# Optimization experiments

Measured on AMD Instinct MI355X. Metric: run time of the kernel, lower is better.

Reference implementation:

```python
import jax, jax.numpy as jnp
import numpy as np

D_MODEL = 1024
D_STATE = 16
D_CONV = 4
EXPAND = 2
D_INNER = EXPAND * D_MODEL          # 2048
DT_RANK = (D_MODEL + 15) // 16      # 64 = ceil(d_model/16)
B, L = 1, 2048


def setup_inputs() -> dict:
    key = jax.random.key(0)
    ks = jax.random.split(key, 8)
    s = lambda fan_in: 1.0 / np.sqrt(fan_in)
    x = jax.random.normal(ks[0], (B, L, D_MODEL), dtype=jnp.float32)
    in_proj_w = jax.random.normal(ks[1], (2 * D_INNER, D_MODEL), dtype=jnp.float32) * s(D_MODEL)
    conv_w = jax.random.normal(ks[2], (D_INNER, 1, D_CONV), dtype=jnp.float32) * s(D_CONV)
    conv_b = jax.random.normal(ks[3], (D_INNER,), dtype=jnp.float32) * s(D_CONV)
    x_proj_w = jax.random.normal(ks[4], (DT_RANK + 2 * D_STATE, D_INNER), dtype=jnp.float32) * s(D_INNER)
    dt_proj_w = jax.random.normal(ks[5], (D_INNER, DT_RANK), dtype=jnp.float32) * s(DT_RANK)
    dt_proj_b = jax.random.normal(ks[6], (D_INNER,), dtype=jnp.float32) * s(DT_RANK)
    A_log = jnp.log(jnp.arange(1, D_STATE + 1, dtype=jnp.float32))[None, :] * jnp.ones((D_INNER, 1), jnp.float32)
    D_param = jnp.ones((D_INNER,), dtype=jnp.float32)
    out_proj_w = jax.random.normal(ks[7], (D_MODEL, D_INNER), dtype=jnp.float32) * s(D_INNER)
    return {"x": x, "in_proj_w": in_proj_w, "conv_w": conv_w, "conv_b": conv_b,
            "x_proj_w": x_proj_w, "dt_proj_w": dt_proj_w, "dt_proj_b": dt_proj_b,
            "A_log": A_log, "D_param": D_param, "out_proj_w": out_proj_w}


def _silu(v):
    return v * jax.nn.sigmoid(v)


def _mamba_fwd(x, in_proj_w, conv_w, conv_b, x_proj_w, dt_proj_w, dt_proj_b, A_log, D_param, out_proj_w):
    b, l, _ = x.shape
    d_state = A_log.shape[1]
    dt_rank = dt_proj_w.shape[1]
    # input projection and gate split
    xz = x @ in_proj_w.T                         # [B, L, 2*d_inner]
    x_inner, z = jnp.split(xz, 2, axis=-1)
    # causal depthwise conv (torch pads both sides then slices [:L] -> left pad only)
    x_c = jax.lax.conv_general_dilated(
        x_inner.transpose(0, 2, 1), conv_w,
        window_strides=(1,), padding=[(conv_w.shape[-1] - 1, 0)],
        feature_group_count=x_inner.shape[-1],
        dimension_numbers=('NCH', 'OIH', 'NCH'))
    x_conv = _silu((x_c + conv_b[None, :, None]).transpose(0, 2, 1))   # [B, L, d_inner]
    # SSM parameterization
    x_dbl = x_conv @ x_proj_w.T                  # [B, L, dt_rank + 2*d_state]
    dt_lr = x_dbl[..., :dt_rank]
    B_ssm = x_dbl[..., dt_rank:dt_rank + d_state]            # [B, L, n]
    C_ssm = x_dbl[..., dt_rank + d_state:]                   # [B, L, n]
    dt = jax.nn.softplus(dt_lr @ dt_proj_w.T + dt_proj_b)    # [B, L, d_inner]
    A = -jnp.exp(A_log)                                      # [d_inner, n]
    dA = jnp.exp(jnp.einsum('bld,dn->bldn', dt, A))          # [B, L, d_inner, n]
    dBx = jnp.einsum('bld,bln->bldn', dt * x_conv, B_ssm)    # dB * x_conv
    # selective scan over time
    def step(h, inp):
        a_t, bx_t, c_t = inp                                 # [B,d,n], [B,d,n], [B,n]
        h = a_t * h + bx_t
        y_t = jnp.einsum('bdn,bn->bd', h, c_t)
        return h, y_t
    h0 = jnp.zeros((b, x_conv.shape[-1], d_state), dtype=x.dtype)
    _, ys = jax.lax.scan(step, h0,
                         (dA.transpose(1, 0, 2, 3), dBx.transpose(1, 0, 2, 3),
                          C_ssm.transpose(1, 0, 2)))
    y = ys.transpose(1, 0, 2) + x_conv * D_param             # [B, L, d_inner]
    return (y * _silu(z)) @ out_proj_w.T                     # [B, L, d_model]


def reference(x, in_proj_w, conv_w, conv_b, x_proj_w, dt_proj_w, dt_proj_b, A_log, D_param, out_proj_w):
    return _mamba_fwd(x, in_proj_w, conv_w, conv_b, x_proj_w, dt_proj_w, dt_proj_b, A_log, D_param, out_proj_w)
```

## Files before the change

### kernel.cpp

```cpp
#include <hip/hip_runtime.h>

#define L_SEQ   2048
#define DMODEL  1024
#define DINNER  2048
#define DSTATE  16
#define RANK    64
#define NPROJ   96
#define NPAD    128
#define XZDIM   4096
#define CHUNK   32
#define NCHUNK  64
#define SPLITK  8

typedef __bf16 bf16x8 __attribute__((ext_vector_type(8)));
typedef float  f32x4  __attribute__((ext_vector_type(4)));

__device__ __forceinline__ unsigned short f2bf(float f) {
  unsigned int x = __float_as_uint(f);
  x += 0x7FFF + ((x >> 16) & 1);
  return (unsigned short)(x >> 16);
}

#define GLD16(g, l)                                                            \
  __builtin_amdgcn_global_load_lds(                                            \
      (const __attribute__((address_space(1))) void*)(g),                      \
      (__attribute__((address_space(3))) void*)(l), 16, 0, 0)

__global__ __launch_bounds__(256) void f32_to_bf16_kernel(
    const float* __restrict__ src, unsigned short* __restrict__ dst) {
  size_t i = ((size_t)blockIdx.x * 256 + threadIdx.x) * 8;
  float4 v0 = *(const float4*)(src + i);
  float4 v1 = *(const float4*)(src + i + 4);
  unsigned short o[8];
  o[0] = f2bf(v0.x); o[1] = f2bf(v0.y); o[2] = f2bf(v0.z); o[3] = f2bf(v0.w);
  o[4] = f2bf(v1.x); o[5] = f2bf(v1.y); o[6] = f2bf(v1.z); o[7] = f2bf(v1.w);
  *(ushort4*)(dst + i)     = make_ushort4(o[0], o[1], o[2], o[3]);
  *(ushort4*)(dst + i + 4) = make_ushort4(o[4], o[5], o[6], o[7]);
}

__global__ __launch_bounds__(256) void pad_convert_xw_kernel(
    const float* __restrict__ src, unsigned short* __restrict__ dst) {
  size_t i = ((size_t)blockIdx.x * 256 + threadIdx.x) * 8;
  int row = (int)(i >> 11);
  unsigned short o[8];
  if (row < NPROJ) {
    float4 v0 = *(const float4*)(src + i);
    float4 v1 = *(const float4*)(src + i + 4);
    o[0] = f2bf(v0.x); o[1] = f2bf(v0.y); o[2] = f2bf(v0.z); o[3] = f2bf(v0.w);
    o[4] = f2bf(v1.x); o[5] = f2bf(v1.y); o[6] = f2bf(v1.z); o[7] = f2bf(v1.w);
  } else {
    for (int t = 0; t < 8; t++) o[t] = 0;
  }
  *(ushort4*)(dst + i)     = make_ushort4(o[0], o[1], o[2], o[3]);
  *(ushort4*)(dst + i + 4) = make_ushort4(o[4], o[5], o[6], o[7]);
}

template <int BM, int BN, int WM, int WN>
__global__ __launch_bounds__(256) void gemm_tile(
    const unsigned short* __restrict__ A, const unsigned short* __restrict__ B,
    float* __restrict__ C, int M, int N, int K) {
  constexpr int WGN = BN / WN;
  constexpr int FM = WM / 16, FN = WN / 16;
  constexpr int CA = BM * 4 / 256;
  constexpr int CB = BN * 4 / 256;
  __shared__ unsigned short As[BM * 32];
  __shared__ unsigned short Bs[BN * 32];
  const int tid  = threadIdx.x;
  const int lane = tid & 63;
  const int wave = tid >> 6;
  const int wr = wave / WGN, wc = wave % WGN;
  const int fr = lane & 15;
  const int kq = (lane >> 4) * 8;
  const size_t bm = blockIdx.y, bn = blockIdx.x;

  f32x4 acc[FM][FN] = {};

  const unsigned short* aptr[CA];
  const unsigned short* bptr[CB];
#pragma unroll
  for (int i = 0; i < CA; i++) {
    int q = tid + i * 256;
    aptr[i] = A + (bm * BM + (q >> 2)) * (size_t)K + (q & 3) * 8;
  }
#pragma unroll
  for (int i = 0; i < CB; i++) {
    int q = tid + i * 256;
    bptr[i] = B + (bn * BN + (q >> 2)) * (size_t)K + (q & 3) * 8;
  }

  for (int k0 = 0; k0 < K; k0 += 32) {
#pragma unroll
    for (int i = 0; i < CA; i++) GLD16(aptr[i] + k0, &As[(tid + i * 256) * 8]);
#pragma unroll
    for (int i = 0; i < CB; i++) GLD16(bptr[i] + k0, &Bs[(tid + i * 256) * 8]);
    __syncthreads();
    bf16x8 af[FM], bg[FN];
#pragma unroll
    for (int m = 0; m < FM; m++)
      af[m] = *(const bf16x8*)&As[(wr * WM + m * 16 + fr) * 32 + kq];
#pragma unroll
    for (int n = 0; n < FN; n++)
      bg[n] = *(const bf16x8*)&Bs[(wc * WN + n * 16 + fr) * 32 + kq];
#pragma unroll
    for (int m = 0; m < FM; m++)
#pragma unroll
      for (int n = 0; n < FN; n++)
        acc[m][n] = __builtin_amdgcn_mfma_f32_16x16x32_bf16(af[m], bg[n],
                                                            acc[m][n], 0, 0, 0);
    __syncthreads();
  }
  const int cr = (lane >> 4) * 4;
#pragma unroll
  for (int m = 0; m < FM; m++)
#pragma unroll
    for (int n = 0; n < FN; n++) {
      float* cp = C + (bm * BM + wr * WM + m * 16 + cr) * (size_t)N +
                  bn * BN + wc * WN + n * 16 + fr;
#pragma unroll
      for (int r = 0; r < 4; r++) cp[(size_t)r * N] = acc[m][n][r];
    }
}

__global__ __launch_bounds__(256) void gemm_dt64_bf16(
    const unsigned short* __restrict__ A,
    const unsigned short* __restrict__ B,
    const float* __restrict__ bias,
    float* __restrict__ dt) {
  __shared__ unsigned short As[64 * 32];
  __shared__ unsigned short Bs[64 * 32];
  const int K = RANK;
  const int tid  = threadIdx.x;
  const int lane = tid & 63;
  const int wave = tid >> 6;
  const int wr = wave >> 1, wc = wave & 1;
  const int fr = lane & 15;
  const int kq = (lane >> 4) * 8;
  const size_t bm = blockIdx.y, bn = blockIdx.x;

  f32x4 acc[2][2] = {};

  const unsigned short* a0 = A + (bm * 64 + (tid >> 2)) * (size_t)K + (tid & 3) * 8;
  const unsigned short* b0 = B + (bn * 64 + (tid >> 2)) * (size_t)K + (tid & 3) * 8;

  for (int k0 = 0; k0 < K; k0 += 32) {
    GLD16(a0 + k0, &As[tid * 8]);
    GLD16(b0 + k0, &Bs[tid * 8]);
    __syncthreads();
    bf16x8 af[2], bg[2];
#pragma unroll
    for (int m = 0; m < 2; m++)
      af[m] = *(const bf16x8*)&As[(wr * 32 + m * 16 + fr) * 32 + kq];
#pragma unroll
    for (int n = 0; n < 2; n++)
      bg[n] = *(const bf16x8*)&Bs[(wc * 32 + n * 16 + fr) * 32 + kq];
#pragma unroll
    for (int m = 0; m < 2; m++)
#pragma unroll
      for (int n = 0; n < 2; n++)
        acc[m][n] = __builtin_amdgcn_mfma_f32_16x16x32_bf16(af[m], bg[n],
                                                            acc[m][n], 0, 0, 0);
    __syncthreads();
  }
  const int cr = (lane >> 4) * 4;
#pragma unroll
  for (int n = 0; n < 2; n++) {
    int col = (int)bn * 64 + wc * 32 + n * 16 + fr;
    float bv = bias[col];
#pragma unroll
    for (int m = 0; m < 2; m++) {
      float* cp = dt + ((size_t)bm * 64 + wr * 32 + m * 16 + cr) * DINNER + col;
#pragma unroll
      for (int r = 0; r < 4; r++) {
        float a = acc[m][n][r] + bv;
        float sp = (a > 20.f) ? a : __logf(1.f + __expf(a));
        cp[(size_t)r * DINNER] = sp;
      }
    }
  }
}

__global__ __launch_bounds__(256) void gemm_xdbl_splitk(
    const unsigned short* __restrict__ A, const unsigned short* __restrict__ B,
    float* __restrict__ Cp) {
  __shared__ unsigned short As[128 * 32];
  __shared__ unsigned short Bs[128 * 32];
  const int K = DINNER;
  const int tid  = threadIdx.x;
  const int lane = tid & 63;
  const int wave = tid >> 6;
  const int wr = wave >> 1, wc = wave & 1;
  const int fr = lane & 15;
  const int kq = (lane >> 4) * 8;
  const int s = blockIdx.x;
  const size_t bm = blockIdx.y;

  f32x4 acc[4][4] = {};

  const int q0 = tid, q1 = tid + 256;
  const unsigned short* a0 = A + (bm * 128 + (q0 >> 2)) * (size_t)K + (q0 & 3) * 8;
  const unsigned short* a1 = A + (bm * 128 + (q1 >> 2)) * (size_t)K + (q1 & 3) * 8;
  const unsigned short* b0 = B + ((size_t)(q0 >> 2)) * K + (q0 & 3) * 8;
  const unsigned short* b1 = B + ((size_t)(q1 >> 2)) * K + (q1 & 3) * 8;

  const int kbeg = s * (DINNER / SPLITK), kend = kbeg + DINNER / SPLITK;
  for (int k0 = kbeg; k0 < kend; k0 += 32) {
    GLD16(a0 + k0, &As[q0 * 8]);
    GLD16(a1 + k0, &As[q1 * 8]);
    GLD16(b0 + k0, &Bs[q0 * 8]);
    GLD16(b1 + k0, &Bs[q1 * 8]);
    __syncthreads();
    bf16x8 af[4], bg[4];
#pragma unroll
    for (int m = 0; m < 4; m++)
      af[m] = *(const bf16x8*)&As[(wr * 64 + m * 16 + fr) * 32 + kq];
#pragma unroll
    for (int n = 0; n < 4; n++)
      bg[n] = *(const bf16x8*)&Bs[(wc * 64 + n * 16 + fr) * 32 + kq];
#pragma unroll
    for (int m = 0; m < 4; m++)
#pragma unroll
      for (int n = 0; n < 4; n++)
        acc[m][n] = __builtin_amdgcn_mfma_f32_16x16x32_bf16(af[m], bg[n],
                                                            acc[m][n], 0, 0, 0);
    __syncthreads();
  }
  const int cr = (lane >> 4) * 4;
  float* Cs = Cp + (size_t)s * L_SEQ * NPAD;
#pragma unroll
  for (int m = 0; m < 4; m++)
#pragma unroll
    for (int n = 0; n < 4; n++) {
      float* cp = Cs + (bm * 128 + wr * 64 + m * 16 + cr) * (size_t)NPAD +
                  wc * 64 + n * 16 + fr;
#pragma unroll
      for (int r = 0; r < 4; r++) cp[(size_t)r * NPAD] = acc[m][n][r];
    }
}

__global__ __launch_bounds__(256) void xdbl_reduce_kernel(
    const float* __restrict__ Cp, float* __restrict__ xdbl,
    unsigned short* __restrict__ dtlr_bf) {
  int i = blockIdx.x * 256 + threadIdx.x;
  int l = i / NPROJ, j = i - l * NPROJ;
  float s = 0.f;
#pragma unroll
  for (int t = 0; t < SPLITK; t++)
    s += Cp[((size_t)t * L_SEQ + l) * NPAD + j];
  xdbl[i] = s;
  if (j < RANK) dtlr_bf[(size_t)l * RANK + j] = f2bf(s);
}

__global__ void conv_silu_kernel(const float* __restrict__ xz,
                                 const float* __restrict__ w,
                                 const float* __restrict__ b,
                                 float* __restrict__ xconv,
                                 unsigned short* __restrict__ xconv_bf) {
  int idx = blockIdx.x * 256 + threadIdx.x;
  int d = idx & (DINNER - 1);
  int l = idx >> 11;
  float4 wv = *(const float4*)(w + (size_t)d * 4);
  float wa[4] = {wv.x, wv.y, wv.z, wv.w};
  float acc = b[d];
#pragma unroll
  for (int t = 0; t < 4; t++) {
    int ll = l - 3 + t;
    if (ll >= 0) acc += xz[(size_t)ll * XZDIM + d] * wa[t];
  }
  float s = acc / (1.0f + __expf(-acc));
  xconv[idx] = s;
  xconv_bf[idx] = f2bf(s);
}

__global__ __launch_bounds__(256) void scan_a_kernel(
    const float* __restrict__ dt, const float* __restrict__ xconv,
    const float* __restrict__ xdbl, const float* __restrict__ A_log,
    float* __restrict__ Pout, float* __restrict__ Hout) {
  __shared__ float Bsm[CHUNK][DSTATE];
  int c = blockIdx.x;
  int d = blockIdx.y * 256 + threadIdx.x;
  for (int i = threadIdx.x; i < CHUNK * DSTATE; i += 256) {
    int l = i >> 4, n = i & 15;
    Bsm[l][n] = xdbl[(size_t)(c * CHUNK + l) * NPROJ + RANK + n];
  }
  __syncthreads();
  float a[16], h[16], P[16];
  const float4* al4 = (const float4*)(A_log + (size_t)d * 16);
#pragma unroll
  for (int q = 0; q < 4; q++) {
    float4 v = al4[q];
    a[q * 4 + 0] = -__expf(v.x); a[q * 4 + 1] = -__expf(v.y);
    a[q * 4 + 2] = -__expf(v.z); a[q * 4 + 3] = -__expf(v.w);
  }
#pragma unroll
  for (int n = 0; n < 16; n++) { h[n] = 0.f; P[n] = 1.f; }
  for (int l = 0; l < CHUNK; l++) {
    int gl = c * CHUNK + l;
    float dtv = dt[(size_t)gl * DINNER + d];
    float xv = xconv[(size_t)gl * DINNER + d];
    float dtx = dtv * xv;
#pragma unroll
    for (int n = 0; n < 16; n++) {
      float dA = __expf(dtv * a[n]);
      P[n] *= dA;
      h[n] = dA * h[n] + dtx * Bsm[l][n];
    }
  }
#pragma unroll
  for (int n = 0; n < 16; n++) {
    size_t o = ((size_t)c * 16 + n) * DINNER + d;
    Pout[o] = P[n];
    Hout[o] = h[n];
  }
}

__global__ void combine_kernel(const float* __restrict__ P,
                               const float* __restrict__ Hl,
                               float* __restrict__ H0) {
  int i = blockIdx.x * 256 + threadIdx.x;
  float h = 0.f;
  for (int c = 0; c < NCHUNK; c++) {
    size_t o = (size_t)c * (DINNER * DSTATE) + i;
    H0[o] = h;
    h = P[o] * h + Hl[o];
  }
}

__global__ __launch_bounds__(256) void scan_c_kernel(
    const float* __restrict__ dt, const float* __restrict__ xconv,
    const float* __restrict__ xdbl, const float* __restrict__ A_log,
    const float* __restrict__ H0, const float* __restrict__ xz,
    const float* __restrict__ Dp, unsigned short* __restrict__ yzbf) {
  __shared__ float Bsm[CHUNK][DSTATE];
  __shared__ float Csm[CHUNK][DSTATE];
  int c = blockIdx.x;
  int d = blockIdx.y * 256 + threadIdx.x;
  for (int i = threadIdx.x; i < CHUNK * DSTATE; i += 256) {
    int l = i >> 4, n = i & 15;
    size_t base = (size_t)(c * CHUNK + l) * NPROJ + RANK;
    Bsm[l][n] = xdbl[base + n];
    Csm[l][n] = xdbl[base + DSTATE + n];
  }
  __syncthreads();
  float a[16], h[16];
  const float4* al4 = (const float4*)(A_log + (size_t)d * 16);
#pragma unroll
  for (int q = 0; q < 4; q++) {
    float4 v = al4[q];
    a[q * 4 + 0] = -__expf(v.x); a[q * 4 + 1] = -__expf(v.y);
    a[q * 4 + 2] = -__expf(v.z); a[q * 4 + 3] = -__expf(v.w);
  }
#pragma unroll
  for (int n = 0; n < 16; n++)
    h[n] = H0[(size_t)c * (DINNER * DSTATE) + n * DINNER + d];
  float dp = Dp[d];
  for (int l = 0; l < CHUNK; l++) {
    int gl = c * CHUNK + l;
    float dtv = dt[(size_t)gl * DINNER + d];
    float xv = xconv[(size_t)gl * DINNER + d];
    float dtx = dtv * xv;
    float y = 0.f;
#pragma unroll
    for (int n = 0; n < 16; n++) {
      float dA = __expf(dtv * a[n]);
      h[n] = dA * h[n] + dtx * Bsm[l][n];
      y += h[n] * Csm[l][n];
    }
    y += xv * dp;
    float zv = xz[(size_t)gl * XZDIM + DINNER + d];
    float sz = zv / (1.0f + __expf(-zv));
    yzbf[(size_t)gl * DINNER + d] = f2bf(y * sz);
  }
}

extern "C" void kernel_launch(void* const* d_in, const int* in_sizes, int n_in,
                              void* d_out, int out_size, void* d_ws, size_t ws_size,
                              hipStream_t stream) {
  const float* x          = (const float*)d_in[0];
  const float* in_proj_w  = (const float*)d_in[1];
  const float* conv_w     = (const float*)d_in[2];
  const float* conv_b     = (const float*)d_in[3];
  const float* x_proj_w   = (const float*)d_in[4];
  const float* dt_proj_w  = (const float*)d_in[5];
  const float* dt_proj_b  = (const float*)d_in[6];
  const float* A_log      = (const float*)d_in[7];
  const float* D_param    = (const float*)d_in[8];
  const float* out_proj_w = (const float*)d_in[9];
  float* out = (float*)d_out;

  float* ws = (float*)d_ws;
  float* xz    = ws;
  float* xconv = xz    + (size_t)L_SEQ * XZDIM;
  float* xdbl  = xconv + (size_t)L_SEQ * DINNER;
  float* dt    = xdbl  + (size_t)L_SEQ * NPROJ;
  float* P     = dt    + (size_t)L_SEQ * DINNER;
  float* Hl    = P     + (size_t)NCHUNK * DINNER * DSTATE;
  float* H0    = Hl    + (size_t)NCHUNK * DINNER * DSTATE;
  float* Cpart = H0    + (size_t)NCHUNK * DINNER * DSTATE;
  unsigned short* bf = (unsigned short*)(Cpart + (size_t)SPLITK * L_SEQ * NPAD);
  unsigned short* x_bf     = bf;
  unsigned short* win_bf   = x_bf     + (size_t)L_SEQ * DMODEL;
  unsigned short* wout_bf  = win_bf   + (size_t)XZDIM * DMODEL;
  unsigned short* yz_bf    = wout_bf  + (size_t)DMODEL * DINNER;
  unsigned short* xconv_bf = yz_bf    + (size_t)L_SEQ * DINNER;
  unsigned short* wpad_bf  = xconv_bf + (size_t)L_SEQ * DINNER;
  unsigned short* dtlr_bf  = wpad_bf  + (size_t)NPAD * DINNER;
  unsigned short* dtw_bf   = dtlr_bf  + (size_t)L_SEQ * RANK;

  f32_to_bf16_kernel<<<(L_SEQ * DMODEL) / 2048, 256, 0, stream>>>(x, x_bf);
  f32_to_bf16_kernel<<<(XZDIM * DMODEL) / 2048, 256, 0, stream>>>(in_proj_w, win_bf);
  f32_to_bf16_kernel<<<(DMODEL * DINNER) / 2048, 256, 0, stream>>>(out_proj_w, wout_bf);
  f32_to_bf16_kernel<<<(DINNER * RANK) / 2048, 256, 0, stream>>>(dt_proj_w, dtw_bf);
  pad_convert_xw_kernel<<<(NPAD * DINNER) / 2048, 256, 0, stream>>>(x_proj_w, wpad_bf);

  gemm_tile<64, 128, 64, 32><<<dim3(XZDIM / 128, L_SEQ / 64), 256, 0, stream>>>(
      x_bf, win_bf, xz, L_SEQ, XZDIM, DMODEL);
  conv_silu_kernel<<<(L_SEQ * DINNER) / 256, 256, 0, stream>>>(
      xz, conv_w, conv_b, xconv, xconv_bf);
  gemm_xdbl_splitk<<<dim3(SPLITK, L_SEQ / 128), 256, 0, stream>>>(
      xconv_bf, wpad_bf, Cpart);
  xdbl_reduce_kernel<<<(L_SEQ * NPROJ) / 256, 256, 0, stream>>>(
      Cpart, xdbl, dtlr_bf);
  gemm_dt64_bf16<<<dim3(DINNER / 64, L_SEQ / 64), 256, 0, stream>>>(
      dtlr_bf, dtw_bf, dt_proj_b, dt);
  scan_a_kernel<<<dim3(NCHUNK, DINNER / 256), 256, 0, stream>>>(
      dt, xconv, xdbl, A_log, P, Hl);
  combine_kernel<<<(DINNER * DSTATE) / 256, 256, 0, stream>>>(P, Hl, H0);
  scan_c_kernel<<<dim3(NCHUNK, DINNER / 256), 256, 0, stream>>>(
      dt, xconv, xdbl, A_log, H0, xz, D_param, yz_bf);
  gemm_tile<64, 64, 32, 32><<<dim3(DMODEL / 64, L_SEQ / 64), 256, 0, stream>>>(
      yz_bf, wout_bf, out, L_SEQ, DMODEL, DINNER);
}
```

Measured before the change: 253.0 us.

## Double-buffer GEMM LDS tiles, fuse weight conversions, raise split-K to 16

The tiled GEMM now uses two LDS buffers and prefetches the next K-slice while running MFMAs on the current one, so global-load latency can overlap with compute. Four separate fp32-to-bf16 conversion launches are merged into one kernel that picks its source by block index, cutting launch overhead. The split-K factor for the x_proj GEMM doubles to 16, which gives more parallel blocks but more partial sums to reduce and a larger workspace. Double buffering doubles LDS use per block, which may lower occupancy.

```diff
diff --git a/kernel.cpp b/kernel.cpp
--- a/kernel.cpp
+++ b/kernel.cpp
@@ -10,7 +10,7 @@
 #define XZDIM   4096
 #define CHUNK   32
 #define NCHUNK  64
-#define SPLITK  8
+#define SPLITK  16
 
 typedef __bf16 bf16x8 __attribute__((ext_vector_type(8)));
 typedef float  f32x4  __attribute__((ext_vector_type(4)));
@@ -26,9 +26,18 @@
       (const __attribute__((address_space(1))) void*)(g),                      \
       (__attribute__((address_space(3))) void*)(l), 16, 0, 0)
 
-__global__ __launch_bounds__(256) void f32_to_bf16_kernel(
-    const float* __restrict__ src, unsigned short* __restrict__ dst) {
-  size_t i = ((size_t)blockIdx.x * 256 + threadIdx.x) * 8;
+__global__ __launch_bounds__(256) void convert_all_kernel(
+    const float* __restrict__ s0, unsigned short* __restrict__ d0,
+    const float* __restrict__ s1, unsigned short* __restrict__ d1,
+    const float* __restrict__ s2, unsigned short* __restrict__ d2,
+    const float* __restrict__ s3, unsigned short* __restrict__ d3) {
+  int b = blockIdx.x;
+  const float* src; unsigned short* dst; size_t base;
+  if (b < 1024)      { src = s0; dst = d0; base = (size_t)b * 2048; }
+  else if (b < 3072) { src = s1; dst = d1; base = (size_t)(b - 1024) * 2048; }
+  else if (b < 4096) { src = s2; dst = d2; base = (size_t)(b - 3072) * 2048; }
+  else               { src = s3; dst = d3; base = (size_t)(b - 4096) * 2048; }
+  size_t i = base + (size_t)threadIdx.x * 8;
   float4 v0 = *(const float4*)(src + i);
   float4 v1 = *(const float4*)(src + i + 4);
   unsigned short o[8];
@@ -63,8 +72,8 @@
   constexpr int FM = WM / 16, FN = WN / 16;
   constexpr int CA = BM * 4 / 256;
   constexpr int CB = BN * 4 / 256;
-  __shared__ unsigned short As[BM * 32];
-  __shared__ unsigned short Bs[BN * 32];
+  __shared__ unsigned short As[2][BM * 32];
+  __shared__ unsigned short Bs[2][BN * 32];
   const int tid  = threadIdx.x;
   const int lane = tid & 63;
   const int wave = tid >> 6;
@@ -88,19 +97,31 @@
     bptr[i] = B + (bn * BN + (q >> 2)) * (size_t)K + (q & 3) * 8;
   }
 
-  for (int k0 = 0; k0 < K; k0 += 32) {
-#pragma unroll
-    for (int i = 0; i < CA; i++) GLD16(aptr[i] + k0, &As[(tid + i * 256) * 8]);
-#pragma unroll
-    for (int i = 0; i < CB; i++) GLD16(bptr[i] + k0, &Bs[(tid + i * 256) * 8]);
-    __syncthreads();
+  const int NT = K / 32;
+#pragma unroll
+  for (int i = 0; i < CA; i++) GLD16(aptr[i], &As[0][(tid + i * 256) * 8]);
+#pragma unroll
+  for (int i = 0; i < CB; i++) GLD16(bptr[i], &Bs[0][(tid + i * 256) * 8]);
+  __syncthreads();
+
+  int cur = 0;
+  for (int t = 0; t < NT; t++) {
+    if (t + 1 < NT) {
+      int nk = (t + 1) * 32;
+#pragma unroll
+      for (int i = 0; i < CA; i++)
+        GLD16(aptr[i] + nk, &As[cur ^ 1][(tid + i * 256) * 8]);
+#pragma unroll
+      for (int i = 0; i < CB; i++)
+        GLD16(bptr[i] + nk, &Bs[cur ^ 1][(tid + i * 256) * 8]);
+    }
     bf16x8 af[FM], bg[FN];
 #pragma unroll
     for (int m = 0; m < FM; m++)
-      af[m] = *(const bf16x8*)&As[(wr * WM + m * 16 + fr) * 32 + kq];
+      af[m] = *(const bf16x8*)&As[cur][(wr * WM + m * 16 + fr) * 32 + kq];
 #pragma unroll
     for (int n = 0; n < FN; n++)
-      bg[n] = *(const bf16x8*)&Bs[(wc * WN + n * 16 + fr) * 32 + kq];
+      bg[n] = *(const bf16x8*)&Bs[cur][(wc * WN + n * 16 + fr) * 32 + kq];
 #pragma unroll
     for (int m = 0; m < FM; m++)
 #pragma unroll
@@ -108,6 +129,7 @@
         acc[m][n] = __builtin_amdgcn_mfma_f32_16x16x32_bf16(af[m], bg[n],
                                                             acc[m][n], 0, 0, 0);
     __syncthreads();
+    cur ^= 1;
   }
   const int cr = (lane >> 4) * 4;
 #pragma unroll
@@ -406,11 +428,10 @@
   unsigned short* dtlr_bf  = wpad_bf  + (size_t)NPAD * DINNER;
   unsigned short* dtw_bf   = dtlr_bf  + (size_t)L_SEQ * RANK;
 
-  f32_to_bf16_kernel<<<(L_SEQ * DMODEL) / 2048, 256, 0, stream>>>(x, x_bf);
-  f32_to_bf16_kernel<<<(XZDIM * DMODEL) / 2048, 256, 0, stream>>>(in_proj_w, win_bf);
-  f32_to_bf16_kernel<<<(DMODEL * DINNER) / 2048, 256, 0, stream>>>(out_proj_w, wout_bf);
-  f32_to_bf16_kernel<<<(DINNER * RANK) / 2048, 256, 0, stream>>>(dt_proj_w, dtw_bf);
-  pad_convert_xw_kernel<<<(NPAD * DINNER) / 2048, 256, 0, stream>>>(x_proj_w, wpad_bf);
+  convert_all_kernel<<<4160, 256, 0, stream>>>(
+      x, x_bf, in_proj_w, win_bf, out_proj_w, wout_bf, dt_proj_w, dtw_bf);
+  pad_convert_xw_kernel<<<(NPAD * DINNER) / 2048, 256, 0, stream>>>(
+      x_proj_w, wpad_bf);
 
   gemm_tile<64, 128, 64, 32><<<dim3(XZDIM / 128, L_SEQ / 64), 256, 0, stream>>>(
       x_bf, win_bf, xz, L_SEQ, XZDIM, DMODEL);
```

New measurement: 245.9 us. -2.8%, faster.
